# Performance work log

Hardware: AMD Instinct MI355X
Metric: run time of the kernel (lower is better)

Reference implementation:

```python
import jax, jax.numpy as jnp
import numpy as np

D, H, T, O = 512, 2048, 2048, 512  # input_dim, hidden_dim, seq_len, output_dim


def _lstm_layer(x, Wih, Whh, bih, bhh):
    """x: (T, Din). Returns (ys: (T, H), h_last: (H,)). PyTorch gate order i,f,g,o."""
    Hd = Whh.shape[1]
    # Hoist the input projection out of the recurrence (one big GEMM).
    x_proj = x @ Wih.T + (bih + bhh)  # (T, 4H)

    def step(carry, xp):
        h, c = carry
        z = xp + h @ Whh.T  # (4H,)
        i, f, g, o = jnp.split(z, 4)
        i = jax.nn.sigmoid(i)
        f = jax.nn.sigmoid(f)
        g = jnp.tanh(g)
        o = jax.nn.sigmoid(o)
        c = f * c + i * g
        h = o * jnp.tanh(c)
        return (h, c), h

    init = (jnp.zeros((Hd,), x.dtype), jnp.zeros((Hd,), x.dtype))
    (h_last, _), ys = jax.lax.scan(step, init, x_proj)
    return ys, h_last


def setup_inputs() -> dict:
    key = jax.random.key(0)
    ks = jax.random.split(key, 12)
    s = 1.0 / np.sqrt(H)  # PyTorch nn.LSTM init: U(-1/sqrt(H), 1/sqrt(H))
    u = lambda k, shape: jax.random.uniform(k, shape, jnp.float32, -s, s)
    return {
        "x": jax.random.normal(ks[0], (1, T, D), jnp.float32),
        "Wih0": u(ks[1], (4 * H, D)),
        "Whh0": u(ks[2], (4 * H, H)),
        "bih0": u(ks[3], (4 * H,)),
        "bhh0": u(ks[4], (4 * H,)),
        "Wih1": u(ks[5], (4 * H, H)),
        "Whh1": u(ks[6], (4 * H, H)),
        "bih1": u(ks[7], (4 * H,)),
        "bhh1": u(ks[8], (4 * H,)),
        "fc_w": u(ks[9], (O, H)),
        "fc_b": u(ks[10], (O,)),
    }


def reference(x, Wih0, Whh0, bih0, bhh0, Wih1, Whh1, bih1, bhh1, fc_w, fc_b):
    xs = x[0]  # (T, D), batch=1
    ys0, _ = _lstm_layer(xs, Wih0, Whh0, bih0, bhh0)
    _, h1 = _lstm_layer(ys0, Wih1, Whh1, bih1, bhh1)  # h_n of last layer
    out = h1 @ fc_w.T + fc_b  # (O,)
    return out[None, :]  # (1, O)
```

## Files before the change

kernel.cpp:

```cpp
#include <hip/hip_runtime.h>
#include <cstdint>

#define H_DIM 2048
#define H4_DIM 8192
#define T_LEN 2048
#define NREP 8

typedef unsigned long long u64;
typedef __attribute__((ext_vector_type(2))) float v2f;

__device__ __forceinline__ float sigmoid_f(float x) {
  return 1.0f / (1.0f + __expf(-x));
}
__device__ __forceinline__ float tanh_f(float x) {
  float ax = fabsf(x);
  float e = __expf(-2.0f * ax);
  float r = (1.0f - e) / (1.0f + e);
  return copysignf(r, x);
}

__global__ __launch_bounds__(512, 2) void lstm_rec(
    const float* __restrict__ Whh,
    const float* __restrict__ xp,
    u64* __restrict__ slots,
    float* __restrict__ ys,
    int T)
{
  __shared__ float hl[H_DIM];
  const int g = blockIdx.x;
  const int tid = threadIdx.x;
  const int w = tid >> 6;
  const int l = tid & 63;
  const int j = g * 8 + w;
  const int rep = g & (NREP - 1);

  v2f wreg[64];
  #pragma unroll
  for (int q = 0; q < 4; ++q) {
    const float* wr = Whh + (size_t)(j + q * H_DIM) * H_DIM + l * 4;
    #pragma unroll
    for (int k = 0; k < 8; ++k) {
      float4 v = *(const float4*)(wr + 256 * k);
      v2f lo; lo.x = v.x; lo.y = v.y;
      v2f hi; hi.x = v.z; hi.y = v.w;
      wreg[q * 16 + k * 2 + 0] = lo;
      wreg[q * 16 + k * 2 + 1] = hi;
    }
  }

  float c = 0.0f;

  for (int t = 0; t < T; ++t) {
    float xq0 = 0.f, xq1 = 0.f, xq2 = 0.f, xq3 = 0.f;
    if (l < NREP) {
      const float* xrow = xp + (size_t)t * H4_DIM + j;
      xq0 = xrow[0];
      xq1 = xrow[H_DIM];
      xq2 = xrow[2 * H_DIM];
      xq3 = xrow[3 * H_DIM];
    }

    if (t == 0) {
      ((float4*)hl)[tid] = make_float4(0.f, 0.f, 0.f, 0.f);
    } else {
      const u64* S = slots + ((size_t)(rep * 2 + (t & 1))) * H_DIM + tid;
      u64 v0, v1, v2, v3;
      for (;;) {
        v0 = __hip_atomic_load(S, __ATOMIC_RELAXED, __HIP_MEMORY_SCOPE_AGENT);
        v1 = __hip_atomic_load(S + 512, __ATOMIC_RELAXED, __HIP_MEMORY_SCOPE_AGENT);
        v2 = __hip_atomic_load(S + 1024, __ATOMIC_RELAXED, __HIP_MEMORY_SCOPE_AGENT);
        v3 = __hip_atomic_load(S + 1536, __ATOMIC_RELAXED, __HIP_MEMORY_SCOPE_AGENT);
        bool ok = ((unsigned)(v0 >> 32) == (unsigned)t) &
                  ((unsigned)(v1 >> 32) == (unsigned)t) &
                  ((unsigned)(v2 >> 32) == (unsigned)t) &
                  ((unsigned)(v3 >> 32) == (unsigned)t);
        if (__all(ok)) break;
        __builtin_amdgcn_s_sleep(1);
      }
      hl[tid]        = __uint_as_float((unsigned)v0);
      hl[tid + 512]  = __uint_as_float((unsigned)v1);
      hl[tid + 1024] = __uint_as_float((unsigned)v2);
      hl[tid + 1536] = __uint_as_float((unsigned)v3);
    }
    __syncthreads();

    v2f a0 = {0.f, 0.f}, a1 = {0.f, 0.f}, a2 = {0.f, 0.f}, a3 = {0.f, 0.f};
    #pragma unroll
    for (int k = 0; k < 8; ++k) {
      float4 h4 = ((const float4*)hl)[l + 64 * k];
      v2f hlo; hlo.x = h4.x; hlo.y = h4.y;
      v2f hhi; hhi.x = h4.z; hhi.y = h4.w;
      a0 = __builtin_elementwise_fma(wreg[0 + k * 2], hlo, a0);
      a0 = __builtin_elementwise_fma(wreg[1 + k * 2], hhi, a0);
      a1 = __builtin_elementwise_fma(wreg[16 + k * 2], hlo, a1);
      a1 = __builtin_elementwise_fma(wreg[17 + k * 2], hhi, a1);
      a2 = __builtin_elementwise_fma(wreg[32 + k * 2], hlo, a2);
      a2 = __builtin_elementwise_fma(wreg[33 + k * 2], hhi, a2);
      a3 = __builtin_elementwise_fma(wreg[48 + k * 2], hlo, a3);
      a3 = __builtin_elementwise_fma(wreg[49 + k * 2], hhi, a3);
    }
    float acc0 = a0.x + a0.y;
    float acc1 = a1.x + a1.y;
    float acc2 = a2.x + a2.y;
    float acc3 = a3.x + a3.y;

    #pragma unroll
    for (int off = 32; off; off >>= 1) {
      acc0 += __shfl_xor(acc0, off);
      acc1 += __shfl_xor(acc1, off);
      acc2 += __shfl_xor(acc2, off);
      acc3 += __shfl_xor(acc3, off);
    }

    float i_ = sigmoid_f(acc0 + xq0);
    float f_ = sigmoid_f(acc1 + xq1);
    float g_ = tanh_f(acc2 + xq2);
    float o_ = sigmoid_f(acc3 + xq3);
    c = f_ * c + i_ * g_;
    float h_ = o_ * tanh_f(c);

    if (l < NREP) {
      union { float f; unsigned u; } cv;
      cv.f = h_;
      u64 pv = ((u64)(unsigned)(t + 1) << 32) | (u64)cv.u;
      __hip_atomic_store(
          slots + ((size_t)(l * 2 + ((t + 1) & 1))) * H_DIM + j, pv,
          __ATOMIC_RELAXED, __HIP_MEMORY_SCOPE_AGENT);
      if (l == 0 && ys) ys[(size_t)t * H_DIM + j] = h_;
    }
    __syncthreads();
  }
}

__global__ __launch_bounds__(256) void gemm_bt_bias(
    const float* __restrict__ A, const float* __restrict__ W,
    const float* __restrict__ b0, const float* __restrict__ b1,
    float* __restrict__ C, int M, int N, int K)
{
  __shared__ float As[8][128];
  __shared__ float Bs[8][128];
  const int tid = threadIdx.x;
  const int n0 = blockIdx.x * 128;
  const int m0 = blockIdx.y * 128;
  const int tx = tid & 15;
  const int ty = tid >> 4;
  const int lr = tid >> 1;
  const int lk = (tid & 1) * 4;
  const float* Ap = A + (size_t)(m0 + lr) * K + lk;
  const float* Wp = W + (size_t)(n0 + lr) * K + lk;

  float acc[8][8];
  #pragma unroll
  for (int i = 0; i < 8; ++i)
    #pragma unroll
    for (int jj = 0; jj < 8; ++jj) acc[i][jj] = 0.f;

  for (int kt = 0; kt < K; kt += 8) {
    float4 av = *(const float4*)(Ap + kt);
    float4 wv = *(const float4*)(Wp + kt);
    __syncthreads();
    As[lk + 0][lr] = av.x; As[lk + 1][lr] = av.y;
    As[lk + 2][lr] = av.z; As[lk + 3][lr] = av.w;
    Bs[lk + 0][lr] = wv.x; Bs[lk + 1][lr] = wv.y;
    Bs[lk + 2][lr] = wv.z; Bs[lk + 3][lr] = wv.w;
    __syncthreads();
    #pragma unroll
    for (int k = 0; k < 8; ++k) {
      float a[8], b[8];
      *(float4*)&a[0] = *(const float4*)&As[k][ty * 8];
      *(float4*)&a[4] = *(const float4*)&As[k][ty * 8 + 4];
      *(float4*)&b[0] = *(const float4*)&Bs[k][tx * 8];
      *(float4*)&b[4] = *(const float4*)&Bs[k][tx * 8 + 4];
      #pragma unroll
      for (int i = 0; i < 8; ++i)
        #pragma unroll
        for (int jj = 0; jj < 8; ++jj)
          acc[i][jj] = fmaf(a[i], b[jj], acc[i][jj]);
    }
  }

  const int n = n0 + tx * 8;
  float bias[8];
  #pragma unroll
  for (int jj = 0; jj < 8; ++jj)
    bias[jj] = b0[n + jj] + (b1 ? b1[n + jj] : 0.f);
  #pragma unroll
  for (int i = 0; i < 8; ++i) {
    float* crow = C + (size_t)(m0 + ty * 8 + i) * N + n;
    float4 v0 = make_float4(acc[i][0] + bias[0], acc[i][1] + bias[1],
                            acc[i][2] + bias[2], acc[i][3] + bias[3]);
    float4 v1 = make_float4(acc[i][4] + bias[4], acc[i][5] + bias[5],
                            acc[i][6] + bias[6], acc[i][7] + bias[7]);
    *(float4*)crow = v0;
    *(float4*)(crow + 4) = v1;
  }
}

__global__ void fc_kernel(const u64* __restrict__ hslots,
                          const float* __restrict__ Wf,
                          const float* __restrict__ bf,
                          float* __restrict__ out)
{
  const int o = blockIdx.x;
  const int l = threadIdx.x;
  const float* wr = Wf + (size_t)o * H_DIM;
  float s = 0.f;
  #pragma unroll
  for (int k = 0; k < 32; ++k) {
    union { unsigned u; float f; } cv;
    cv.u = (unsigned)hslots[l + 64 * k];
    s = fmaf(wr[l + 64 * k], cv.f, s);
  }
  #pragma unroll
  for (int off = 32; off; off >>= 1) s += __shfl_xor(s, off);
  if (l == 0) out[o] = s + bf[o];
}

extern "C" void kernel_launch(void* const* d_in, const int* in_sizes, int n_in,
                              void* d_out, int out_size, void* d_ws, size_t ws_size,
                              hipStream_t stream) {
  const float* x    = (const float*)d_in[0];
  const float* Wih0 = (const float*)d_in[1];
  const float* Whh0 = (const float*)d_in[2];
  const float* bih0 = (const float*)d_in[3];
  const float* bhh0 = (const float*)d_in[4];
  const float* Wih1 = (const float*)d_in[5];
  const float* Whh1 = (const float*)d_in[6];
  const float* bih1 = (const float*)d_in[7];
  const float* bhh1 = (const float*)d_in[8];
  const float* fcw  = (const float*)d_in[9];
  const float* fcb  = (const float*)d_in[10];
  float* out = (float*)d_out;

  float* ws   = (float*)d_ws;
  float* xp   = ws;
  float* ys   = ws + 16777216;
  u64* slots0 = (u64*)(ws + 20971520);
  u64* slots1 = slots0 + NREP * 2 * H_DIM;

  dim3 gblk(256);
  dim3 ggrid(H4_DIM / 128, T_LEN / 128);

  gemm_bt_bias<<<ggrid, gblk, 0, stream>>>(x, Wih0, bih0, bhh0, xp,
                                           T_LEN, H4_DIM, 512);
  lstm_rec<<<256, 512, 0, stream>>>(Whh0, xp, slots0, ys, T_LEN);

  gemm_bt_bias<<<ggrid, gblk, 0, stream>>>(ys, Wih1, bih1, bhh1, xp,
                                           T_LEN, H4_DIM, H_DIM);
  lstm_rec<<<256, 512, 0, stream>>>(Whh1, xp, slots1, nullptr, T_LEN);

  fc_kernel<<<512, 64, 0, stream>>>(slots1, fcw, fcb, out);
}
```

Before: 11.21 ms.

## Fuse both LSTM layers into one wavefront-pipelined persistent recurrence kernel

Merges the layer-0 and layer-1 recurrences into one persistent kernel. At step r it computes layer-0 step r and layer-1 step r-1, so layer 1 consumes h0 directly. The input projection for layer 1 is computed inside the loop using Wih1 weights held in registers. This removes the second input-projection GEMM, the ys round-trip through memory and one full 2048-step serial recurrence. The cost is that each block now holds three register-resident weight slices instead of one, under the same launch bounds. That may force heavy register spilling and longer per-step latency, and each step also has to poll two sets of flags.

```diff
diff --git a/kernel.cpp b/kernel.cpp
--- a/kernel.cpp
+++ b/kernel.cpp
@@ -19,14 +19,19 @@
   return copysignf(r, x);
 }
 
-__global__ __launch_bounds__(512, 2) void lstm_rec(
-    const float* __restrict__ Whh,
+__global__ __launch_bounds__(512, 2) void lstm_fused(
+    const float* __restrict__ Whh0,
+    const float* __restrict__ Wih1,
+    const float* __restrict__ Whh1,
     const float* __restrict__ xp,
-    u64* __restrict__ slots,
-    float* __restrict__ ys,
+    const float* __restrict__ bih1,
+    const float* __restrict__ bhh1,
+    u64* __restrict__ slots0,
+    u64* __restrict__ slots1,
     int T)
 {
-  __shared__ float hl[H_DIM];
+  __shared__ float hl0[H_DIM];
+  __shared__ float hl1[H_DIM];
   const int g = blockIdx.x;
   const int tid = threadIdx.x;
   const int w = tid >> 6;
@@ -34,99 +39,163 @@
   const int j = g * 8 + w;
   const int rep = g & (NREP - 1);
 
-  v2f wreg[64];
+  v2f w0r[64], wi1r[64], wh1r[64];
   #pragma unroll
   for (int q = 0; q < 4; ++q) {
-    const float* wr = Whh + (size_t)(j + q * H_DIM) * H_DIM + l * 4;
+    const size_t row = (size_t)(j + q * H_DIM) * H_DIM + l * 4;
+    const float* p0 = Whh0 + row;
+    const float* p1 = Wih1 + row;
+    const float* p2 = Whh1 + row;
     #pragma unroll
     for (int k = 0; k < 8; ++k) {
-      float4 v = *(const float4*)(wr + 256 * k);
-      v2f lo; lo.x = v.x; lo.y = v.y;
-      v2f hi; hi.x = v.z; hi.y = v.w;
-      wreg[q * 16 + k * 2 + 0] = lo;
-      wreg[q * 16 + k * 2 + 1] = hi;
-    }
-  }
-
-  float c = 0.0f;
-
-  for (int t = 0; t < T; ++t) {
+      float4 v0 = *(const float4*)(p0 + 256 * k);
+      float4 v1 = *(const float4*)(p1 + 256 * k);
+      float4 v2 = *(const float4*)(p2 + 256 * k);
+      w0r [q * 16 + k * 2 + 0] = (v2f){v0.x, v0.y};
+      w0r [q * 16 + k * 2 + 1] = (v2f){v0.z, v0.w};
+      wi1r[q * 16 + k * 2 + 0] = (v2f){v1.x, v1.y};
+      wi1r[q * 16 + k * 2 + 1] = (v2f){v1.z, v1.w};
+      wh1r[q * 16 + k * 2 + 0] = (v2f){v2.x, v2.y};
+      wh1r[q * 16 + k * 2 + 1] = (v2f){v2.z, v2.w};
+    }
+  }
+  const float bi1_0 = bih1[j]             + bhh1[j];
+  const float bi1_1 = bih1[j + H_DIM]     + bhh1[j + H_DIM];
+  const float bi1_2 = bih1[j + 2 * H_DIM] + bhh1[j + 2 * H_DIM];
+  const float bi1_3 = bih1[j + 3 * H_DIM] + bhh1[j + 3 * H_DIM];
+
+  float c0 = 0.0f, c1 = 0.0f;
+
+  for (int r = 0; r <= T; ++r) {
     float xq0 = 0.f, xq1 = 0.f, xq2 = 0.f, xq3 = 0.f;
-    if (l < NREP) {
-      const float* xrow = xp + (size_t)t * H4_DIM + j;
+    if (r < T && l < NREP) {
+      const float* xrow = xp + (size_t)r * H4_DIM + j;
       xq0 = xrow[0];
       xq1 = xrow[H_DIM];
       xq2 = xrow[2 * H_DIM];
       xq3 = xrow[3 * H_DIM];
     }
 
-    if (t == 0) {
-      ((float4*)hl)[tid] = make_float4(0.f, 0.f, 0.f, 0.f);
+    if (r == 0) {
+      ((float4*)hl0)[tid] = make_float4(0.f, 0.f, 0.f, 0.f);
+      ((float4*)hl1)[tid] = make_float4(0.f, 0.f, 0.f, 0.f);
     } else {
-      const u64* S = slots + ((size_t)(rep * 2 + (t & 1))) * H_DIM + tid;
-      u64 v0, v1, v2, v3;
+      const u64* S0 = slots0 + (size_t)(rep * 2 + (r & 1)) * H_DIM + tid;
+      const u64* S1 = slots1 + (size_t)(rep * 2 + (r & 1)) * H_DIM + tid;
+      u64 u0, u1, u2, u3, q0, q1, q2, q3;
       for (;;) {
-        v0 = __hip_atomic_load(S, __ATOMIC_RELAXED, __HIP_MEMORY_SCOPE_AGENT);
-        v1 = __hip_atomic_load(S + 512, __ATOMIC_RELAXED, __HIP_MEMORY_SCOPE_AGENT);
-        v2 = __hip_atomic_load(S + 1024, __ATOMIC_RELAXED, __HIP_MEMORY_SCOPE_AGENT);
-        v3 = __hip_atomic_load(S + 1536, __ATOMIC_RELAXED, __HIP_MEMORY_SCOPE_AGENT);
-        bool ok = ((unsigned)(v0 >> 32) == (unsigned)t) &
-                  ((unsigned)(v1 >> 32) == (unsigned)t) &
-                  ((unsigned)(v2 >> 32) == (unsigned)t) &
-                  ((unsigned)(v3 >> 32) == (unsigned)t);
+        u0 = __hip_atomic_load(S0,        __ATOMIC_RELAXED, __HIP_MEMORY_SCOPE_AGENT);
+        u1 = __hip_atomic_load(S0 + 512,  __ATOMIC_RELAXED, __HIP_MEMORY_SCOPE_AGENT);
+        u2 = __hip_atomic_load(S0 + 1024, __ATOMIC_RELAXED, __HIP_MEMORY_SCOPE_AGENT);
+        u3 = __hip_atomic_load(S0 + 1536, __ATOMIC_RELAXED, __HIP_MEMORY_SCOPE_AGENT);
+        q0 = __hip_atomic_load(S1,        __ATOMIC_RELAXED, __HIP_MEMORY_SCOPE_AGENT);
+        q1 = __hip_atomic_load(S1 + 512,  __ATOMIC_RELAXED, __HIP_MEMORY_SCOPE_AGENT);
+        q2 = __hip_atomic_load(S1 + 1024, __ATOMIC_RELAXED, __HIP_MEMORY_SCOPE_AGENT);
+        q3 = __hip_atomic_load(S1 + 1536, __ATOMIC_RELAXED, __HIP_MEMORY_SCOPE_AGENT);
+        bool ok = ((unsigned)(u0 >> 32) == (unsigned)r) &
+                  ((unsigned)(u1 >> 32) == (unsigned)r) &
+                  ((unsigned)(u2 >> 32) == (unsigned)r) &
+                  ((unsigned)(u3 >> 32) == (unsigned)r) &
+                  ((unsigned)(q0 >> 32) == (unsigned)r) &
+                  ((unsigned)(q1 >> 32) == (unsigned)r) &
+                  ((unsigned)(q2 >> 32) == (unsigned)r) &
+                  ((unsigned)(q3 >> 32) == (unsigned)r);
         if (__all(ok)) break;
         __builtin_amdgcn_s_sleep(1);
       }
-      hl[tid]        = __uint_as_float((unsigned)v0);
-      hl[tid + 512]  = __uint_as_float((unsigned)v1);
-      hl[tid + 1024] = __uint_as_float((unsigned)v2);
-      hl[tid + 1536] = __uint_as_float((unsigned)v3);
+      hl0[tid]        = __uint_as_float((unsigned)u0);
+      hl0[tid + 512]  = __uint_as_float((unsigned)u1);
+      hl0[tid + 1024] = __uint_as_float((unsigned)u2);
+      hl0[tid + 1536] = __uint_as_float((unsigned)u3);
+      hl1[tid]        = __uint_as_float((unsigned)q0);
+      hl1[tid + 512]  = __uint_as_float((unsigned)q1);
+      hl1[tid + 1024] = __uint_as_float((unsigned)q2);
+      hl1[tid + 1536] = __uint_as_float((unsigned)q3);
     }
     __syncthreads();
 
-    v2f a0 = {0.f, 0.f}, a1 = {0.f, 0.f}, a2 = {0.f, 0.f}, a3 = {0.f, 0.f};
+    v2f A0 = {0.f, 0.f}, A1 = {0.f, 0.f}, A2 = {0.f, 0.f}, A3 = {0.f, 0.f};
+    v2f B0 = {0.f, 0.f}, B1 = {0.f, 0.f}, B2 = {0.f, 0.f}, B3 = {0.f, 0.f};
     #pragma unroll
     for (int k = 0; k < 8; ++k) {
-      float4 h4 = ((const float4*)hl)[l + 64 * k];
-      v2f hlo; hlo.x = h4.x; hlo.y = h4.y;
-      v2f hhi; hhi.x = h4.z; hhi.y = h4.w;
-      a0 = __builtin_elementwise_fma(wreg[0 + k * 2], hlo, a0);
-      a0 = __builtin_elementwise_fma(wreg[1 + k * 2], hhi, a0);
-      a1 = __builtin_elementwise_fma(wreg[16 + k * 2], hlo, a1);
-      a1 = __builtin_elementwise_fma(wreg[17 + k * 2], hhi, a1);
-      a2 = __builtin_elementwise_fma(wreg[32 + k * 2], hlo, a2);
-      a2 = __builtin_elementwise_fma(wreg[33 + k * 2], hhi, a2);
-      a3 = __builtin_elementwise_fma(wreg[48 + k * 2], hlo, a3);
-      a3 = __builtin_elementwise_fma(wreg[49 + k * 2], hhi, a3);
-    }
-    float acc0 = a0.x + a0.y;
-    float acc1 = a1.x + a1.y;
-    float acc2 = a2.x + a2.y;
-    float acc3 = a3.x + a3.y;
+      float4 h04 = ((const float4*)hl0)[l + 64 * k];
+      float4 h14 = ((const float4*)hl1)[l + 64 * k];
+      v2f h0lo = {h04.x, h04.y}, h0hi = {h04.z, h04.w};
+      v2f h1lo = {h14.x, h14.y}, h1hi = {h14.z, h14.w};
+      A0 = __builtin_elementwise_fma(w0r[0 + k * 2],  h0lo, A0);
+      A0 = __builtin_elementwise_fma(w0r[1 + k * 2],  h0hi, A0);
+      A1 = __builtin_elementwise_fma(w0r[16 + k * 2], h0lo, A1);
+      A1 = __builtin_elementwise_fma(w0r[17 + k * 2], h0hi, A1);
+      A2 = __builtin_elementwise_fma(w0r[32 + k * 2], h0lo, A2);
+      A2 = __builtin_elementwise_fma(w0r[33 + k * 2], h0hi, A2);
+      A3 = __builtin_elementwise_fma(w0r[48 + k * 2], h0lo, A3);
+      A3 = __builtin_elementwise_fma(w0r[49 + k * 2], h0hi, A3);
+
+      B0 = __builtin_elementwise_fma(wi1r[0 + k * 2],  h0lo, B0);
+      B0 = __builtin_elementwise_fma(wi1r[1 + k * 2],  h0hi, B0);
+      B1 = __builtin_elementwise_fma(wi1r[16 + k * 2], h0lo, B1);
+      B1 = __builtin_elementwise_fma(wi1r[17 + k * 2], h0hi, B1);
+      B2 = __builtin_elementwise_fma(wi1r[32 + k * 2], h0lo, B2);
+      B2 = __builtin_elementwise_fma(wi1r[33 + k * 2], h0hi, B2);
+      B3 = __builtin_elementwise_fma(wi1r[48 + k * 2], h0lo, B3);
+      B3 = __builtin_elementwise_fma(wi1r[49 + k * 2], h0hi, B3);
+
+      B0 = __builtin_elementwise_fma(wh1r[0 + k * 2],  h1lo, B0);
+      B0 = __builtin_elementwise_fma(wh1r[1 + k * 2],  h1hi, B0);
+      B1 = __builtin_elementwise_fma(wh1r[16 + k * 2], h1lo, B1);
+      B1 = __builtin_elementwise_fma(wh1r[17 + k * 2], h1hi, B1);
+      B2 = __builtin_elementwise_fma(wh1r[32 + k * 2], h1lo, B2);
+      B2 = __builtin_elementwise_fma(wh1r[33 + k * 2], h1hi, B2);
+      B3 = __builtin_elementwise_fma(wh1r[48 + k * 2], h1lo, B3);
+      B3 = __builtin_elementwise_fma(wh1r[49 + k * 2], h1hi, B3);
+    }
+    float a0 = A0.x + A0.y, a1 = A1.x + A1.y;
+    float a2 = A2.x + A2.y, a3 = A3.x + A3.y;
+    float b0 = B0.x + B0.y, b1 = B1.x + B1.y;
+    float b2 = B2.x + B2.y, b3 = B3.x + B3.y;
 
     #pragma unroll
     for (int off = 32; off; off >>= 1) {
-      acc0 += __shfl_xor(acc0, off);
-      acc1 += __shfl_xor(acc1, off);
-      acc2 += __shfl_xor(acc2, off);
-      acc3 += __shfl_xor(acc3, off);
-    }
-
-    float i_ = sigmoid_f(acc0 + xq0);
-    float f_ = sigmoid_f(acc1 + xq1);
-    float g_ = tanh_f(acc2 + xq2);
-    float o_ = sigmoid_f(acc3 + xq3);
-    c = f_ * c + i_ * g_;
-    float h_ = o_ * tanh_f(c);
+      a0 += __shfl_xor(a0, off);
+      a1 += __shfl_xor(a1, off);
+      a2 += __shfl_xor(a2, off);
+      a3 += __shfl_xor(a3, off);
+      b0 += __shfl_xor(b0, off);
+      b1 += __shfl_xor(b1, off);
+      b2 += __shfl_xor(b2, off);
+      b3 += __shfl_xor(b3, off);
+    }
+
+    float h0_ = 0.f;
+    if (r < T) {
+      float i_ = sigmoid_f(a0 + xq0);
+      float f_ = sigmoid_f(a1 + xq1);
+      float g_ = tanh_f(a2 + xq2);
+      float o_ = sigmoid_f(a3 + xq3);
+      c0 = f_ * c0 + i_ * g_;
+      h0_ = o_ * tanh_f(c0);
+    }
+    float h1_ = 0.f;
+    if (r >= 1) {
+      float i_ = sigmoid_f(b0 + bi1_0);
+      float f_ = sigmoid_f(b1 + bi1_1);
+      float g_ = tanh_f(b2 + bi1_2);
+      float o_ = sigmoid_f(b3 + bi1_3);
+      c1 = f_ * c1 + i_ * g_;
+      h1_ = o_ * tanh_f(c1);
+    }
 
     if (l < NREP) {
-      union { float f; unsigned u; } cv;
-      cv.f = h_;
-      u64 pv = ((u64)(unsigned)(t + 1) << 32) | (u64)cv.u;
-      __hip_atomic_store(
-          slots + ((size_t)(l * 2 + ((t + 1) & 1))) * H_DIM + j, pv,
-          __ATOMIC_RELAXED, __HIP_MEMORY_SCOPE_AGENT);
-      if (l == 0 && ys) ys[(size_t)t * H_DIM + j] = h_;
+      const size_t soff = (size_t)(l * 2 + ((r + 1) & 1)) * H_DIM + j;
+      const u64 tagw = (u64)(unsigned)(r + 1) << 32;
+      if (r < T) {
+        union { float f; unsigned u; } cv; cv.f = h0_;
+        __hip_atomic_store(slots0 + soff, tagw | (u64)cv.u,
+                           __ATOMIC_RELAXED, __HIP_MEMORY_SCOPE_AGENT);
+      }
+      union { float f; unsigned u; } dv; dv.f = h1_;
+      __hip_atomic_store(slots1 + soff, tagw | (u64)dv.u,
+                         __ATOMIC_RELAXED, __HIP_MEMORY_SCOPE_AGENT);
     }
     __syncthreads();
   }
@@ -234,8 +303,7 @@
 
   float* ws   = (float*)d_ws;
   float* xp   = ws;
-  float* ys   = ws + 16777216;
-  u64* slots0 = (u64*)(ws + 20971520);
+  u64* slots0 = (u64*)(ws + 16777216);
   u64* slots1 = slots0 + NREP * 2 * H_DIM;
 
   dim3 gblk(256);
@@ -243,11 +311,7 @@
 
   gemm_bt_bias<<<ggrid, gblk, 0, stream>>>(x, Wih0, bih0, bhh0, xp,
                                            T_LEN, H4_DIM, 512);
-  lstm_rec<<<256, 512, 0, stream>>>(Whh0, xp, slots0, ys, T_LEN);
-
-  gemm_bt_bias<<<ggrid, gblk, 0, stream>>>(ys, Wih1, bih1, bhh1, xp,
-                                           T_LEN, H4_DIM, H_DIM);
-  lstm_rec<<<256, 512, 0, stream>>>(Whh1, xp, slots1, nullptr, T_LEN);
-
-  fc_kernel<<<512, 64, 0, stream>>>(slots1, fcw, fcb, out);
-}
+  lstm_fused<<<256, 512, 0, stream>>>(Whh0, Wih1, Whh1, xp, bih1, bhh1,
+                                      slots0, slots1, T_LEN);
+  fc_kernel<<<512, 64, 0, stream>>>(slots1 + H_DIM, fcw, fcb, out);
+}
```

New measurement: 43.81 ms. +290.7%, slower.

## Store input projection transposed and prefetch 16 timesteps per wave via shuffles

Applied to the files above, without the earlier changes.

The input-projection GEMM now writes its output transposed (gate-row major, time contiguous). The recurrent kernel then loads 16 consecutive timesteps of all four gates with one load per lane every 16 steps, and broadcasts each step's values with lane shuffles. The aim is to take the per-step strided global load of x_proj off the critical path of the serial recurrence. The cost is a transposed, less coalesced store pattern in the GEMM epilogue and a few extra shuffles per step.

```diff
diff --git a/kernel.cpp b/kernel.cpp
--- a/kernel.cpp
+++ b/kernel.cpp
@@ -48,16 +48,14 @@
     }
   }
 
+  const float* xbase = xp + (size_t)(j + (l >> 4) * H_DIM) * T_LEN + (l & 15);
+
   float c = 0.0f;
+  float pref = 0.0f;
 
   for (int t = 0; t < T; ++t) {
-    float xq0 = 0.f, xq1 = 0.f, xq2 = 0.f, xq3 = 0.f;
-    if (l < NREP) {
-      const float* xrow = xp + (size_t)t * H4_DIM + j;
-      xq0 = xrow[0];
-      xq1 = xrow[H_DIM];
-      xq2 = xrow[2 * H_DIM];
-      xq3 = xrow[3 * H_DIM];
+    if ((t & 15) == 0) {
+      pref = xbase[t];
     }
 
     if (t == 0) {
@@ -112,6 +110,12 @@
       acc3 += __shfl_xor(acc3, off);
     }
 
+    const int dt = t & 15;
+    float xq0 = __shfl(pref, dt);
+    float xq1 = __shfl(pref, 16 + dt);
+    float xq2 = __shfl(pref, 32 + dt);
+    float xq3 = __shfl(pref, 48 + dt);
+
     float i_ = sigmoid_f(acc0 + xq0);
     float f_ = sigmoid_f(acc1 + xq1);
     float g_ = tanh_f(acc2 + xq2);
@@ -132,10 +136,10 @@
   }
 }
 
-__global__ __launch_bounds__(256) void gemm_bt_bias(
+__global__ __launch_bounds__(256) void gemm_bt_bias_T(
     const float* __restrict__ A, const float* __restrict__ W,
     const float* __restrict__ b0, const float* __restrict__ b1,
-    float* __restrict__ C, int M, int N, int K)
+    float* __restrict__ Ct, int M, int N, int K)
 {
   __shared__ float As[8][128];
   __shared__ float Bs[8][128];
@@ -180,17 +184,15 @@
   }
 
   const int n = n0 + tx * 8;
-  float bias[8];
-  #pragma unroll
-  for (int jj = 0; jj < 8; ++jj)
-    bias[jj] = b0[n + jj] + (b1 ? b1[n + jj] : 0.f);
-  #pragma unroll
-  for (int i = 0; i < 8; ++i) {
-    float* crow = C + (size_t)(m0 + ty * 8 + i) * N + n;
-    float4 v0 = make_float4(acc[i][0] + bias[0], acc[i][1] + bias[1],
-                            acc[i][2] + bias[2], acc[i][3] + bias[3]);
-    float4 v1 = make_float4(acc[i][4] + bias[4], acc[i][5] + bias[5],
-                            acc[i][6] + bias[6], acc[i][7] + bias[7]);
+  const int m = m0 + ty * 8;
+  #pragma unroll
+  for (int jj = 0; jj < 8; ++jj) {
+    const float bias = b0[n + jj] + (b1 ? b1[n + jj] : 0.f);
+    float* crow = Ct + (size_t)(n + jj) * M + m;
+    float4 v0 = make_float4(acc[0][jj] + bias, acc[1][jj] + bias,
+                            acc[2][jj] + bias, acc[3][jj] + bias);
+    float4 v1 = make_float4(acc[4][jj] + bias, acc[5][jj] + bias,
+                            acc[6][jj] + bias, acc[7][jj] + bias);
     *(float4*)crow = v0;
     *(float4*)(crow + 4) = v1;
   }
@@ -241,12 +243,12 @@
   dim3 gblk(256);
   dim3 ggrid(H4_DIM / 128, T_LEN / 128);
 
-  gemm_bt_bias<<<ggrid, gblk, 0, stream>>>(x, Wih0, bih0, bhh0, xp,
-                                           T_LEN, H4_DIM, 512);
+  gemm_bt_bias_T<<<ggrid, gblk, 0, stream>>>(x, Wih0, bih0, bhh0, xp,
+                                             T_LEN, H4_DIM, 512);
   lstm_rec<<<256, 512, 0, stream>>>(Whh0, xp, slots0, ys, T_LEN);
 
-  gemm_bt_bias<<<ggrid, gblk, 0, stream>>>(ys, Wih1, bih1, bhh1, xp,
-                                           T_LEN, H4_DIM, H_DIM);
+  gemm_bt_bias_T<<<ggrid, gblk, 0, stream>>>(ys, Wih1, bih1, bhh1, xp,
+                                             T_LEN, H4_DIM, H_DIM);
   lstm_rec<<<256, 512, 0, stream>>>(Whh1, xp, slots1, nullptr, T_LEN);
 
   fc_kernel<<<512, 64, 0, stream>>>(slots1, fcw, fcb, out);
```

New measurement: 14.14 ms. 26.1% more time.
